# Performance work log

Hardware: AMD Instinct MI355X
Metric: run time of the kernel (lower is better)

The kernel has to match this reference:

```python
import jax, jax.numpy as jnp
import numpy as np

N_NODES = 50000
N_EDGES = 800000
BATCH = 4


def setup_inputs() -> dict:
    key = jax.random.key(0)
    ks = jax.random.split(key, 12)
    inp = {
        "x": jax.random.normal(ks[0], (BATCH, N_NODES, 1, 1), dtype=jnp.float32),
        "edge_index": jax.random.randint(ks[1], (2, N_EDGES), 0, N_NODES, dtype=jnp.int64),
        "W_conv1": jax.random.normal(ks[2], (3, 1, 32), dtype=jnp.float32) * 0.1,
        "b_conv1": jnp.zeros((3, 32), dtype=jnp.float32),
        "W_lin1": jax.random.normal(ks[3], (3, 64, 32), dtype=jnp.float32) * 0.1,
        "b_lin1": jnp.zeros((3, 32), dtype=jnp.float32),
        "att1": jax.random.uniform(ks[4], (1,), dtype=jnp.float32),
        "W_conv2": jax.random.normal(ks[5], (3, 32, 32), dtype=jnp.float32) * 0.1,
        "b_conv2": jnp.zeros((3, 32), dtype=jnp.float32),
        "W_lin2": jax.random.normal(ks[6], (3, 64, 32), dtype=jnp.float32) * 0.1,
        "b_lin2": jnp.zeros((3, 32), dtype=jnp.float32),
        "att2": jax.random.uniform(ks[7], (1,), dtype=jnp.float32),
        "W_out": jax.random.normal(ks[8], (32, 1), dtype=jnp.float32) * 0.1,
        "b_out": jnp.zeros((1,), dtype=jnp.float32),
    }
    return inp


def _gcn(h, W, b, src, dst, norm, inv_deg, n):
    # h: (B,N,Fin) -> (B,N,Fout); symmetric-normalized GCNConv with self loops
    xw = h @ W                                   # (B,N,Fout)
    msg = xw[:, src, :] * norm[None, :, None]    # (B,E,Fout)
    agg = jax.ops.segment_sum(jnp.swapaxes(msg, 0, 1), dst, num_segments=n)
    agg = jnp.swapaxes(agg, 0, 1)                # (B,N,Fout)
    return agg + xw * inv_deg[None, :, None] + b


def _tgcn_cell(h_in, Wc, bc, Wl, bl, att, src, dst, norm, inv_deg, n):
    # TGCN2 GRU cell with H0 = 0, weighted by softmax(att) (periods=1 -> weight 1)
    B = h_in.shape[0]
    out_dim = Wc.shape[-1]
    H = jnp.zeros((B, n, out_dim), dtype=h_in.dtype)
    cz = _gcn(h_in, Wc[0], bc[0], src, dst, norm, inv_deg, n)
    Z = jax.nn.sigmoid(jnp.concatenate([cz, H], axis=-1) @ Wl[0] + bl[0])
    cr = _gcn(h_in, Wc[1], bc[1], src, dst, norm, inv_deg, n)
    R = jax.nn.sigmoid(jnp.concatenate([cr, H], axis=-1) @ Wl[1] + bl[1])
    ch = _gcn(h_in, Wc[2], bc[2], src, dst, norm, inv_deg, n)
    Ht = jnp.tanh(jnp.concatenate([ch, H * R], axis=-1) @ Wl[2] + bl[2])
    Hn = Z * H + (1.0 - Z) * Ht
    a = jax.nn.softmax(att)  # (1,) -> [1.0]
    return a[0] * Hn


def reference(x, edge_index, W_conv1, b_conv1, W_lin1, b_lin1, att1,
              W_conv2, b_conv2, W_lin2, b_lin2, att2, W_out, b_out):
    n = x.shape[1]
    src, dst = edge_index[0], edge_index[1]
    ones = jnp.ones(src.shape[0], dtype=x.dtype)
    deg = jax.ops.segment_sum(ones, dst, num_segments=n) + 1.0  # + self loop
    dis = jax.lax.rsqrt(deg)
    norm = dis[src] * dis[dst]   # (E,)
    inv_deg = 1.0 / deg          # self-loop norm

    h = x[..., 0]  # (B,N,1) periods=1
    h = jax.nn.relu(_tgcn_cell(h, W_conv1, b_conv1, W_lin1, b_lin1, att1,
                               src, dst, norm, inv_deg, n))
    h = jax.nn.relu(_tgcn_cell(h, W_conv2, b_conv2, W_lin2, b_lin2, att2,
                               src, dst, norm, inv_deg, n))
    return h @ W_out + b_out  # (B,N,1)
```

## Files before the change

### kernel.cpp

```cpp
#include <hip/hip_runtime.h>
#include <stdint.h>

#define N_NODES 50000
#define BATCH 4
#define CAP 64

__global__ void fill_kernel(const int* __restrict__ src,
                            const int* __restrict__ dst,
                            int* __restrict__ cursor,
                            unsigned short* __restrict__ bucket, int E) {
    int e = blockIdx.x * blockDim.x + threadIdx.x;
    if (e < E) {
        int d = dst[e];
        int pos = atomicAdd(&cursor[d], 1);
        if (pos < CAP) bucket[d * CAP + pos] = (unsigned short)src[e];
    }
}

__global__ void dis_xd_kernel(const int* __restrict__ deg,
                              const float* __restrict__ x,
                              float* __restrict__ dis,
                              float4* __restrict__ xd, int N) {
    int n = blockIdx.x * blockDim.x + threadIdx.x;
    if (n >= N) return;
    float d = rsqrtf((float)(deg[n] + 1));
    dis[n] = d;
    xd[n] = make_float4(x[n] * d, x[N + n] * d, x[2 * N + n] * d,
                        x[3 * N + n] * d);
}

__global__ void precomp_kernel(const float* __restrict__ Wc1,
                               const float* __restrict__ bc1,
                               const float* __restrict__ Wl1,
                               const float* __restrict__ bl1,
                               const float* __restrict__ Wc2,
                               const float* __restrict__ bc2,
                               const float* __restrict__ Wl2,
                               const float* __restrict__ bl2,
                               float* __restrict__ pc) {
    int i = blockIdx.x * blockDim.x + threadIdx.x;
    if (i < 2048) {
        int g = i >> 10;
        int kf = i & 1023;
        int k = kf >> 5, f = kf & 31;
        int gate = g ? 2 : 0;
        float s = 0.0f;
        for (int j = 0; j < 32; ++j)
            s += Wc2[gate * 1024 + k * 32 + j] * Wl2[gate * 2048 + j * 32 + f];
        pc[i] = s;
    } else if (i < 2112) {
        int g = (i - 2048) >> 5;
        int f = i & 31;
        int gate = g ? 2 : 0;
        float s = bl2[gate * 32 + f];
        for (int j = 0; j < 32; ++j)
            s += bc2[gate * 32 + j] * Wl2[gate * 2048 + j * 32 + f];
        pc[i] = s;
    } else if (i < 2240) {
        int t = i - 2112;
        int which = t >> 5;
        int f = t & 31;
        int gate = (which >= 2) ? 2 : 0;
        if ((which & 1) == 0) {
            float s = 0.0f;
            for (int j = 0; j < 32; ++j)
                s += Wc1[gate * 32 + j] * Wl1[gate * 2048 + j * 32 + f];
            pc[i] = s;
        } else {
            float s = bl1[gate * 32 + f];
            for (int j = 0; j < 32; ++j)
                s += bc1[gate * 32 + j] * Wl1[gate * 2048 + j * 32 + f];
            pc[i] = s;
        }
    }
}

__global__ void s1_kernel(const float4* __restrict__ xd,
                          const float* __restrict__ dis,
                          const int* __restrict__ deg,
                          const unsigned short* __restrict__ bucket,
                          float4* __restrict__ t4, int N) {
    int idx = blockIdx.x * blockDim.x + threadIdx.x;
    int node = idx >> 3;
    if (node >= N) return;
    int j = idx & 7;
    int cnt = deg[node];
    if (cnt > CAP) cnt = CAP;
    float4 a;
    if (j == 0) a = xd[node];
    else a = make_float4(0.f, 0.f, 0.f, 0.f);
    for (int i = j; i < cnt; i += 8) {
        int s = bucket[node * CAP + i];
        float4 v = xd[s];
        a.x += v.x; a.y += v.y; a.z += v.z; a.w += v.w;
    }
#pragma unroll
    for (int m = 4; m; m >>= 1) {
        a.x += __shfl_xor(a.x, m, 64);
        a.y += __shfl_xor(a.y, m, 64);
        a.z += __shfl_xor(a.z, m, 64);
        a.w += __shfl_xor(a.w, m, 64);
    }
    if (j == 0) {
        float d = dis[node];
        t4[node] = make_float4(a.x * d, a.y * d, a.z * d, a.w * d);
    }
}

__global__ void h1_kernel(const float4* __restrict__ t4,
                          const float* __restrict__ dis,
                          const float* __restrict__ pc,
                          float4* __restrict__ hs, int N) {
    int idx = blockIdx.x * blockDim.x + threadIdx.x;
    if (idx >= N * 32) return;
    int f = idx & 31;
    int n = idx >> 5;
    float4 t = t4[n];
    float uz = pc[2112 + f], vz = pc[2144 + f];
    float uh = pc[2176 + f], vh = pc[2208 + f];
    float d = dis[n];
    float4 o;
    o.x = fmaxf((1.0f - 1.0f / (1.0f + expf(-(t.x * uz + vz)))) *
                tanhf(t.x * uh + vh), 0.0f) * d;
    o.y = fmaxf((1.0f - 1.0f / (1.0f + expf(-(t.y * uz + vz)))) *
                tanhf(t.y * uh + vh), 0.0f) * d;
    o.z = fmaxf((1.0f - 1.0f / (1.0f + expf(-(t.z * uz + vz)))) *
                tanhf(t.z * uh + vh), 0.0f) * d;
    o.w = fmaxf((1.0f - 1.0f / (1.0f + expf(-(t.w * uz + vz)))) *
                tanhf(t.w * uh + vh), 0.0f) * d;
    hs[idx] = o;
}

__global__ __launch_bounds__(256) void l2_agg_kernel(
    const float* __restrict__ hs, const float* __restrict__ dis,
    const int* __restrict__ deg, const unsigned short* __restrict__ bucket,
    const float* __restrict__ pc, const float* __restrict__ Wout,
    const float* __restrict__ bout, float* __restrict__ out, int N) {
    __shared__ float2 sT[4][64];

    int wv = threadIdx.x >> 6;
    int lane = threadIdx.x & 63;
    int f = lane & 31;
    int h = lane >> 5;

    float wl0[32], wl2[32];
#pragma unroll
    for (int k = 0; k < 32; ++k) {
        wl0[k] = pc[k * 32 + f];
        wl2[k] = pc[1024 + k * 32 + f];
    }
    float w0 = pc[2048 + f], w2 = pc[2080 + f];
    float wf = Wout[f];
    float bo = bout[0];
    const float* hp = hs + f * 4 + h * 2;

    int wid = (blockIdx.x * blockDim.x + threadIdx.x) >> 6;
    int nw = (gridDim.x * blockDim.x) >> 6;

    for (int node = wid; node < N; node += nw) {
        int cnt = deg[node];
        if (cnt > CAP) cnt = CAP;
        int bidx = bucket[node * CAP + lane];
        float2 acc = *(const float2*)(hp + (size_t)node * 128);
        int i = 0;
        for (; i + 8 <= cnt; i += 8) {
            int s0 = __shfl(bidx, i);
            int s1 = __shfl(bidx, i + 1);
            int s2 = __shfl(bidx, i + 2);
            int s3 = __shfl(bidx, i + 3);
            int s4 = __shfl(bidx, i + 4);
            int s5 = __shfl(bidx, i + 5);
            int s6 = __shfl(bidx, i + 6);
            int s7 = __shfl(bidx, i + 7);
            float2 v0 = *(const float2*)(hp + (size_t)s0 * 128);
            float2 v1 = *(const float2*)(hp + (size_t)s1 * 128);
            float2 v2 = *(const float2*)(hp + (size_t)s2 * 128);
            float2 v3 = *(const float2*)(hp + (size_t)s3 * 128);
            float2 v4 = *(const float2*)(hp + (size_t)s4 * 128);
            float2 v5 = *(const float2*)(hp + (size_t)s5 * 128);
            float2 v6 = *(const float2*)(hp + (size_t)s6 * 128);
            float2 v7 = *(const float2*)(hp + (size_t)s7 * 128);
            acc.x += ((v0.x + v1.x) + (v2.x + v3.x)) +
                     ((v4.x + v5.x) + (v6.x + v7.x));
            acc.y += ((v0.y + v1.y) + (v2.y + v3.y)) +
                     ((v4.y + v5.y) + (v6.y + v7.y));
        }
        for (; i < cnt; ++i) {
            int s = __shfl(bidx, i);
            float2 v = *(const float2*)(hp + (size_t)s * 128);
            acc.x += v.x;
            acc.y += v.y;
        }

        sT[wv][lane] = acc;
        asm volatile("s_waitcnt lgkmcnt(0)" ::: "memory");

        float dn = dis[node];
        float sz0 = 0.f, sz1 = 0.f, sh0 = 0.f, sh1 = 0.f;
        const float2* tp = &sT[wv][h * 32];
#pragma unroll
        for (int k = 0; k < 32; k += 2) {
            float4 t2 = *(const float4*)&tp[k];
            sz0 += t2.x * wl0[k];     sz1 += t2.y * wl0[k];
            sh0 += t2.x * wl2[k];     sh1 += t2.y * wl2[k];
            sz0 += t2.z * wl0[k + 1]; sz1 += t2.w * wl0[k + 1];
            sh0 += t2.z * wl2[k + 1]; sh1 += t2.w * wl2[k + 1];
        }
        float z0 = 1.0f / (1.0f + expf(-(dn * sz0 + w0)));
        float z1 = 1.0f / (1.0f + expf(-(dn * sz1 + w0)));
        float t0 = tanhf(dn * sh0 + w2);
        float t1 = tanhf(dn * sh1 + w2);
        float h20 = fmaxf((1.0f - z0) * t0, 0.0f);
        float h21 = fmaxf((1.0f - z1) * t1, 0.0f);

        float o0 = h20 * wf;
        float o1 = h21 * wf;
#pragma unroll
        for (int d = 16; d; d >>= 1) {
            o0 += __shfl_xor(o0, d, 64);
            o1 += __shfl_xor(o1, d, 64);
        }
        if (f == 0) {
            out[(size_t)(2 * h) * N + node] = o0 + bo;
            out[(size_t)(2 * h + 1) * N + node] = o1 + bo;
        }
    }
}


extern "C" void kernel_launch(void* const* d_in, const int* in_sizes, int n_in,
                              void* d_out, int out_size, void* d_ws,
                              size_t ws_size, hipStream_t stream) {
    const float* x    = (const float*)d_in[0];
    const int*   ei   = (const int*)d_in[1];
    const float* Wc1  = (const float*)d_in[2];
    const float* bc1  = (const float*)d_in[3];
    const float* Wl1  = (const float*)d_in[4];
    const float* bl1  = (const float*)d_in[5];
    const float* Wc2  = (const float*)d_in[7];
    const float* bc2  = (const float*)d_in[8];
    const float* Wl2  = (const float*)d_in[9];
    const float* bl2  = (const float*)d_in[10];
    const float* Wout = (const float*)d_in[12];
    const float* bout = (const float*)d_in[13];

    const int E = in_sizes[1] / 2;
    const int N = N_NODES;
    const int* src = ei;
    const int* dst = ei + E;

    char* p = (char*)d_ws;
    auto alloc = [&](size_t bytes) {
        char* r = p;
        p += (bytes + 15) & ~(size_t)15;
        return r;
    };
    int*            cursor = (int*)alloc(N * sizeof(int));
    unsigned short* bucket = (unsigned short*)alloc((size_t)N * CAP * 2);
    float*          dis    = (float*)alloc(N * sizeof(float));
    float*          xd     = (float*)alloc((size_t)N * 4 * sizeof(float));
    float*          t4     = (float*)alloc((size_t)N * 4 * sizeof(float));
    float*          hs     = (float*)alloc((size_t)N * 128 * sizeof(float));
    float*          pc     = (float*)alloc(2240 * sizeof(float));

    hipMemsetAsync(cursor, 0, N * sizeof(int), stream);

    precomp_kernel<<<(2240 + 255) / 256, 256, 0, stream>>>(
        Wc1, bc1, Wl1, bl1, Wc2, bc2, Wl2, bl2, pc);

    fill_kernel<<<(E + 255) / 256, 256, 0, stream>>>(src, dst, cursor, bucket,
                                                     E);
    dis_xd_kernel<<<(N + 255) / 256, 256, 0, stream>>>(cursor, x, dis,
                                                       (float4*)xd, N);

    s1_kernel<<<(N * 8 + 255) / 256, 256, 0, stream>>>(
        (const float4*)xd, dis, cursor, bucket, (float4*)t4, N);
    h1_kernel<<<(N * 32 + 255) / 256, 256, 0, stream>>>(
        (const float4*)t4, dis, pc, (float4*)hs, N);

    l2_agg_kernel<<<1024, 256, 0, stream>>>(hs, dis, cursor, bucket, pc, Wout,
                                            bout, (float*)d_out, N);
}
```

Before: 249.5 us.

## Fuse layer-1 kernels, store hidden state in fp16, use readlane matvec

Merges the s1 and h1 kernels so each node's 8 threads aggregate neighbours and then compute the layer-1 GRU output directly. The intermediate t4 buffer and one launch go away. The layer-1 hidden state is stored as half precision, which halves the bytes gathered per edge in the layer-2 aggregation. The layer-2 kernel replaces the shared-memory transpose with readlane broadcasts, splits the Z and H gates across half-waves, and doubles the grid size. The fp16 storage adds rounding error, and the readlane loop adds scalar-to-vector traffic.

```diff
diff --git a/kernel.cpp b/kernel.cpp
--- a/kernel.cpp
+++ b/kernel.cpp
@@ -1,4 +1,5 @@
 #include <hip/hip_runtime.h>
+#include <hip/hip_fp16.h>
 #include <stdint.h>
 
 #define N_NODES 50000
@@ -75,84 +76,77 @@
     }
 }
 
-__global__ void s1_kernel(const float4* __restrict__ xd,
-                          const float* __restrict__ dis,
-                          const int* __restrict__ deg,
-                          const unsigned short* __restrict__ bucket,
-                          float4* __restrict__ t4, int N) {
+__global__ void s1h1_kernel(const float4* __restrict__ xd,
+                            const float* __restrict__ dis,
+                            const int* __restrict__ deg,
+                            const unsigned short* __restrict__ bucket,
+                            const float* __restrict__ pc,
+                            char* __restrict__ hs, int N) {
     int idx = blockIdx.x * blockDim.x + threadIdx.x;
     int node = idx >> 3;
     if (node >= N) return;
     int j = idx & 7;
     int cnt = deg[node];
     if (cnt > CAP) cnt = CAP;
-    float4 a;
-    if (j == 0) a = xd[node];
-    else a = make_float4(0.f, 0.f, 0.f, 0.f);
+    float ax, ay, az, aw;
+    if (j == 0) {
+        float4 v = xd[node];
+        ax = v.x; ay = v.y; az = v.z; aw = v.w;
+    } else {
+        ax = ay = az = aw = 0.f;
+    }
     for (int i = j; i < cnt; i += 8) {
         int s = bucket[node * CAP + i];
         float4 v = xd[s];
-        a.x += v.x; a.y += v.y; a.z += v.z; a.w += v.w;
+        ax += v.x; ay += v.y; az += v.z; aw += v.w;
     }
 #pragma unroll
     for (int m = 4; m; m >>= 1) {
-        a.x += __shfl_xor(a.x, m, 64);
-        a.y += __shfl_xor(a.y, m, 64);
-        a.z += __shfl_xor(a.z, m, 64);
-        a.w += __shfl_xor(a.w, m, 64);
-    }
-    if (j == 0) {
-        float d = dis[node];
-        t4[node] = make_float4(a.x * d, a.y * d, a.z * d, a.w * d);
-    }
-}
-
-__global__ void h1_kernel(const float4* __restrict__ t4,
-                          const float* __restrict__ dis,
-                          const float* __restrict__ pc,
-                          float4* __restrict__ hs, int N) {
-    int idx = blockIdx.x * blockDim.x + threadIdx.x;
-    if (idx >= N * 32) return;
-    int f = idx & 31;
-    int n = idx >> 5;
-    float4 t = t4[n];
-    float uz = pc[2112 + f], vz = pc[2144 + f];
-    float uh = pc[2176 + f], vh = pc[2208 + f];
-    float d = dis[n];
-    float4 o;
-    o.x = fmaxf((1.0f - 1.0f / (1.0f + expf(-(t.x * uz + vz)))) *
-                tanhf(t.x * uh + vh), 0.0f) * d;
-    o.y = fmaxf((1.0f - 1.0f / (1.0f + expf(-(t.y * uz + vz)))) *
-                tanhf(t.y * uh + vh), 0.0f) * d;
-    o.z = fmaxf((1.0f - 1.0f / (1.0f + expf(-(t.z * uz + vz)))) *
-                tanhf(t.z * uh + vh), 0.0f) * d;
-    o.w = fmaxf((1.0f - 1.0f / (1.0f + expf(-(t.w * uz + vz)))) *
-                tanhf(t.w * uh + vh), 0.0f) * d;
-    hs[idx] = o;
+        ax += __shfl_xor(ax, m, 64);
+        ay += __shfl_xor(ay, m, 64);
+        az += __shfl_xor(az, m, 64);
+        aw += __shfl_xor(aw, m, 64);
+    }
+    float d = dis[node];
+    float t0 = ax * d, t1 = ay * d, t2 = az * d, t3 = aw * d;
+#pragma unroll
+    for (int m = 0; m < 4; ++m) {
+        int f = j + 8 * m;
+        float uz = pc[2112 + f], vz = pc[2144 + f];
+        float uh = pc[2176 + f], vh = pc[2208 + f];
+        float h0 = fmaxf((1.0f - 1.0f / (1.0f + expf(-(t0 * uz + vz)))) *
+                         tanhf(t0 * uh + vh), 0.0f) * d;
+        float h1 = fmaxf((1.0f - 1.0f / (1.0f + expf(-(t1 * uz + vz)))) *
+                         tanhf(t1 * uh + vh), 0.0f) * d;
+        float h2 = fmaxf((1.0f - 1.0f / (1.0f + expf(-(t2 * uz + vz)))) *
+                         tanhf(t2 * uh + vh), 0.0f) * d;
+        float h3 = fmaxf((1.0f - 1.0f / (1.0f + expf(-(t3 * uz + vz)))) *
+                         tanhf(t3 * uh + vh), 0.0f) * d;
+        __half2 lo = __floats2half2_rn(h0, h1);
+        __half2 hi = __floats2half2_rn(h2, h3);
+        uint2 u;
+        u.x = *reinterpret_cast<unsigned int*>(&lo);
+        u.y = *reinterpret_cast<unsigned int*>(&hi);
+        *reinterpret_cast<uint2*>(hs + (size_t)node * 256 + f * 8) = u;
+    }
 }
 
 __global__ __launch_bounds__(256) void l2_agg_kernel(
-    const float* __restrict__ hs, const float* __restrict__ dis,
+    const char* __restrict__ hs, const float* __restrict__ dis,
     const int* __restrict__ deg, const unsigned short* __restrict__ bucket,
     const float* __restrict__ pc, const float* __restrict__ Wout,
     const float* __restrict__ bout, float* __restrict__ out, int N) {
-    __shared__ float2 sT[4][64];
-
-    int wv = threadIdx.x >> 6;
     int lane = threadIdx.x & 63;
     int f = lane & 31;
     int h = lane >> 5;
 
-    float wl0[32], wl2[32];
-#pragma unroll
-    for (int k = 0; k < 32; ++k) {
-        wl0[k] = pc[k * 32 + f];
-        wl2[k] = pc[1024 + k * 32 + f];
-    }
-    float w0 = pc[2048 + f], w2 = pc[2080 + f];
+    float mcol[32];
+#pragma unroll
+    for (int k = 0; k < 32; ++k) mcol[k] = pc[h * 1024 + k * 32 + f];
+    float wv = pc[2048 + h * 32 + f];
     float wf = Wout[f];
     float bo = bout[0];
-    const float* hp = hs + f * 4 + h * 2;
+    const char* hp = hs + f * 8 + h * 4;
 
     int wid = (blockIdx.x * blockDim.x + threadIdx.x) >> 6;
     int nw = (gridDim.x * blockDim.x) >> 6;
@@ -160,69 +154,87 @@
     for (int node = wid; node < N; node += nw) {
         int cnt = deg[node];
         if (cnt > CAP) cnt = CAP;
-        int bidx = bucket[node * CAP + lane];
-        float2 acc = *(const float2*)(hp + (size_t)node * 128);
+        unsigned int bidx = bucket[node * CAP + lane];
+        __half2 sv = *(const __half2*)(hp + (size_t)node * 256);
+        float2 fs = __half22float2(sv);
+        float accx = fs.x, accy = fs.y;
         int i = 0;
         for (; i + 8 <= cnt; i += 8) {
-            int s0 = __shfl(bidx, i);
-            int s1 = __shfl(bidx, i + 1);
-            int s2 = __shfl(bidx, i + 2);
-            int s3 = __shfl(bidx, i + 3);
-            int s4 = __shfl(bidx, i + 4);
-            int s5 = __shfl(bidx, i + 5);
-            int s6 = __shfl(bidx, i + 6);
-            int s7 = __shfl(bidx, i + 7);
-            float2 v0 = *(const float2*)(hp + (size_t)s0 * 128);
-            float2 v1 = *(const float2*)(hp + (size_t)s1 * 128);
-            float2 v2 = *(const float2*)(hp + (size_t)s2 * 128);
-            float2 v3 = *(const float2*)(hp + (size_t)s3 * 128);
-            float2 v4 = *(const float2*)(hp + (size_t)s4 * 128);
-            float2 v5 = *(const float2*)(hp + (size_t)s5 * 128);
-            float2 v6 = *(const float2*)(hp + (size_t)s6 * 128);
-            float2 v7 = *(const float2*)(hp + (size_t)s7 * 128);
-            acc.x += ((v0.x + v1.x) + (v2.x + v3.x)) +
-                     ((v4.x + v5.x) + (v6.x + v7.x));
-            acc.y += ((v0.y + v1.y) + (v2.y + v3.y)) +
-                     ((v4.y + v5.y) + (v6.y + v7.y));
+            unsigned int o0 = __builtin_amdgcn_readlane(bidx, i) * 256u;
+            unsigned int o1 = __builtin_amdgcn_readlane(bidx, i + 1) * 256u;
+            unsigned int o2 = __builtin_amdgcn_readlane(bidx, i + 2) * 256u;
+            unsigned int o3 = __builtin_amdgcn_readlane(bidx, i + 3) * 256u;
+            unsigned int o4 = __builtin_amdgcn_readlane(bidx, i + 4) * 256u;
+            unsigned int o5 = __builtin_amdgcn_readlane(bidx, i + 5) * 256u;
+            unsigned int o6 = __builtin_amdgcn_readlane(bidx, i + 6) * 256u;
+            unsigned int o7 = __builtin_amdgcn_readlane(bidx, i + 7) * 256u;
+            __half2 v0 = *(const __half2*)(hp + o0);
+            __half2 v1 = *(const __half2*)(hp + o1);
+            __half2 v2 = *(const __half2*)(hp + o2);
+            __half2 v3 = *(const __half2*)(hp + o3);
+            __half2 v4 = *(const __half2*)(hp + o4);
+            __half2 v5 = *(const __half2*)(hp + o5);
+            __half2 v6 = *(const __half2*)(hp + o6);
+            __half2 v7 = *(const __half2*)(hp + o7);
+            float2 f0 = __half22float2(v0), f1 = __half22float2(v1);
+            float2 f2 = __half22float2(v2), f3 = __half22float2(v3);
+            float2 f4 = __half22float2(v4), f5 = __half22float2(v5);
+            float2 f6 = __half22float2(v6), f7 = __half22float2(v7);
+            accx += ((f0.x + f1.x) + (f2.x + f3.x)) +
+                    ((f4.x + f5.x) + (f6.x + f7.x));
+            accy += ((f0.y + f1.y) + (f2.y + f3.y)) +
+                    ((f4.y + f5.y) + (f6.y + f7.y));
         }
         for (; i < cnt; ++i) {
-            int s = __shfl(bidx, i);
-            float2 v = *(const float2*)(hp + (size_t)s * 128);
-            acc.x += v.x;
-            acc.y += v.y;
-        }
-
-        sT[wv][lane] = acc;
-        asm volatile("s_waitcnt lgkmcnt(0)" ::: "memory");
-
+            unsigned int o = __builtin_amdgcn_readlane(bidx, i) * 256u;
+            float2 fv = __half22float2(*(const __half2*)(hp + o));
+            accx += fv.x;
+            accy += fv.y;
+        }
+
+        float g0 = 0.f, g1 = 0.f, g2 = 0.f, g3 = 0.f;
+#pragma unroll
+        for (int k = 0; k < 32; ++k) {
+            float tb0 = __int_as_float(
+                __builtin_amdgcn_readlane(__float_as_int(accx), k));
+            float tb1 = __int_as_float(
+                __builtin_amdgcn_readlane(__float_as_int(accy), k));
+            float tb2 = __int_as_float(
+                __builtin_amdgcn_readlane(__float_as_int(accx), 32 + k));
+            float tb3 = __int_as_float(
+                __builtin_amdgcn_readlane(__float_as_int(accy), 32 + k));
+            float m = mcol[k];
+            g0 += tb0 * m; g1 += tb1 * m; g2 += tb2 * m; g3 += tb3 * m;
+        }
         float dn = dis[node];
-        float sz0 = 0.f, sz1 = 0.f, sh0 = 0.f, sh1 = 0.f;
-        const float2* tp = &sT[wv][h * 32];
-#pragma unroll
-        for (int k = 0; k < 32; k += 2) {
-            float4 t2 = *(const float4*)&tp[k];
-            sz0 += t2.x * wl0[k];     sz1 += t2.y * wl0[k];
-            sh0 += t2.x * wl2[k];     sh1 += t2.y * wl2[k];
-            sz0 += t2.z * wl0[k + 1]; sz1 += t2.w * wl0[k + 1];
-            sh0 += t2.z * wl2[k + 1]; sh1 += t2.w * wl2[k + 1];
-        }
-        float z0 = 1.0f / (1.0f + expf(-(dn * sz0 + w0)));
-        float z1 = 1.0f / (1.0f + expf(-(dn * sz1 + w0)));
-        float t0 = tanhf(dn * sh0 + w2);
-        float t1 = tanhf(dn * sh1 + w2);
-        float h20 = fmaxf((1.0f - z0) * t0, 0.0f);
-        float h21 = fmaxf((1.0f - z1) * t1, 0.0f);
-
-        float o0 = h20 * wf;
-        float o1 = h21 * wf;
-#pragma unroll
-        for (int d = 16; d; d >>= 1) {
-            o0 += __shfl_xor(o0, d, 64);
-            o1 += __shfl_xor(o1, d, 64);
-        }
-        if (f == 0) {
-            out[(size_t)(2 * h) * N + node] = o0 + bo;
-            out[(size_t)(2 * h + 1) * N + node] = o1 + bo;
+        float a0 = dn * g0 + wv, a1 = dn * g1 + wv;
+        float a2 = dn * g2 + wv, a3 = dn * g3 + wv;
+        float v0 = h ? tanhf(a0) : 1.0f / (1.0f + expf(-a0));
+        float v1 = h ? tanhf(a1) : 1.0f / (1.0f + expf(-a1));
+        float v2 = h ? tanhf(a2) : 1.0f / (1.0f + expf(-a2));
+        float v3 = h ? tanhf(a3) : 1.0f / (1.0f + expf(-a3));
+        float p0 = __shfl_xor(v0, 32, 64);
+        float p1 = __shfl_xor(v1, 32, 64);
+        float p2 = __shfl_xor(v2, 32, 64);
+        float p3 = __shfl_xor(v3, 32, 64);
+        if (h == 0) {
+            float o0 = fmaxf((1.0f - v0) * p0, 0.0f) * wf;
+            float o1 = fmaxf((1.0f - v1) * p1, 0.0f) * wf;
+            float o2 = fmaxf((1.0f - v2) * p2, 0.0f) * wf;
+            float o3 = fmaxf((1.0f - v3) * p3, 0.0f) * wf;
+#pragma unroll
+            for (int d = 16; d; d >>= 1) {
+                o0 += __shfl_xor(o0, d, 64);
+                o1 += __shfl_xor(o1, d, 64);
+                o2 += __shfl_xor(o2, d, 64);
+                o3 += __shfl_xor(o3, d, 64);
+            }
+            if (f == 0) {
+                out[node] = o0 + bo;
+                out[(size_t)N + node] = o1 + bo;
+                out[(size_t)2 * N + node] = o2 + bo;
+                out[(size_t)3 * N + node] = o3 + bo;
+            }
         }
     }
 }
@@ -259,8 +271,7 @@
     unsigned short* bucket = (unsigned short*)alloc((size_t)N * CAP * 2);
     float*          dis    = (float*)alloc(N * sizeof(float));
     float*          xd     = (float*)alloc((size_t)N * 4 * sizeof(float));
-    float*          t4     = (float*)alloc((size_t)N * 4 * sizeof(float));
-    float*          hs     = (float*)alloc((size_t)N * 128 * sizeof(float));
+    char*           hs     = (char*)alloc((size_t)N * 256);
     float*          pc     = (float*)alloc(2240 * sizeof(float));
 
     hipMemsetAsync(cursor, 0, N * sizeof(int), stream);
@@ -273,11 +284,9 @@
     dis_xd_kernel<<<(N + 255) / 256, 256, 0, stream>>>(cursor, x, dis,
                                                        (float4*)xd, N);
 
-    s1_kernel<<<(N * 8 + 255) / 256, 256, 0, stream>>>(
-        (const float4*)xd, dis, cursor, bucket, (float4*)t4, N);
-    h1_kernel<<<(N * 32 + 255) / 256, 256, 0, stream>>>(
-        (const float4*)t4, dis, pc, (float4*)hs, N);
-
-    l2_agg_kernel<<<1024, 256, 0, stream>>>(hs, dis, cursor, bucket, pc, Wout,
+    s1h1_kernel<<<(N * 8 + 255) / 256, 256, 0, stream>>>(
+        (const float4*)xd, dis, cursor, bucket, pc, hs, N);
+
+    l2_agg_kernel<<<2048, 256, 0, stream>>>(hs, dis, cursor, bucket, pc, Wout,
                                             bout, (float*)d_out, N);
 }
```

After: 218.0 us. -12.6%, faster.
